# Performance work log

Measured on AMD Instinct MI355X. Metric: run time of the kernel, lower is better.

## Reference

```python
import jax, jax.numpy as jnp
import numpy as np


def setup_inputs() -> dict:
    key = jax.random.key(0)
    k1, k2, k3, k4 = jax.random.split(key, 4)
    n_nodes, n_edges, d_in, d_half = 100000, 1600000, 256, 128
    x = jax.random.normal(k1, (n_nodes, d_in), dtype=jnp.float32)
    edge_index = jax.random.randint(k2, (2, n_edges), 0, n_nodes, dtype=jnp.int64)
    W_f = jax.random.normal(k3, (d_half, d_in), dtype=jnp.float32) * (1.0 / np.sqrt(d_in))
    W_b = jax.random.normal(k4, (d_half, d_in), dtype=jnp.float32) * (1.0 / np.sqrt(d_in))
    bias_param = jnp.zeros((2 * d_half,), dtype=jnp.float32)
    return {"x": x, "edge_index": edge_index, "W_f": W_f, "W_b": W_b, "bias_param": bias_param}


def _inv_sqrt(deg):
    # deg.pow(-0.5) with inf -> 0
    return jnp.where(deg > 0, jax.lax.rsqrt(deg), 0.0)


def reference(x, edge_index, W_f, W_b, bias_param):
    n_nodes = x.shape[0]
    # add_remaining_self_loops with fill value 1
    loops = jnp.arange(n_nodes, dtype=edge_index.dtype)
    ei = jnp.concatenate([edge_index, jnp.stack([loops, loops])], axis=1)
    n_e = ei.shape[1]
    w = jnp.ones((n_e,), dtype=x.dtype)
    # directed_norm, flow='source_to_target': col, row = edge_index
    col, row = ei[0], ei[1]
    in_deg = jax.ops.segment_sum(w, col, num_segments=n_nodes)
    out_deg = jax.ops.segment_sum(w, row, num_segments=n_nodes)
    ew = _inv_sqrt(out_deg)[row] * w * _inv_sqrt(in_deg)[col]  # [E]
    # adj_forward: source=row, target=col ; adj_backward: source=col, target=row
    mf = (x @ W_f.T)[row] * ew[:, None]           # [E, d_half]
    y_forward = jax.ops.segment_sum(mf, col, num_segments=n_nodes)
    mb = (x @ W_b.T)[col] * ew[:, None]           # [E, d_half]
    y_backward = jax.ops.segment_sum(mb, row, num_segments=n_nodes)
    y = jnp.concatenate([y_forward, y_backward], axis=-1) + bias_param
    return y
```

## Files before the change

### kernel.cpp

```cpp
#include <hip/hip_runtime.h>

#define D_IN 256
#define D_HALF 128

typedef __attribute__((ext_vector_type(8))) short short8;
typedef __attribute__((ext_vector_type(4))) float float4v;

__device__ __forceinline__ unsigned short f2bf(float f) {
    union { float f; unsigned u; } v; v.f = f;
    unsigned r = v.u + 0x7FFF + ((v.u >> 16) & 1);
    return (unsigned short)(r >> 16);
}
__device__ __forceinline__ float bflo(unsigned u) { union { unsigned u; float f; } v; v.u = u << 16; return v.f; }
__device__ __forceinline__ float bfhi(unsigned u) { union { unsigned u; float f; } v; v.u = u & 0xffff0000u; return v.f; }

__device__ __forceinline__ void async16(const void* g, void* l) {
    __builtin_amdgcn_global_load_lds(
        (const __attribute__((address_space(1))) unsigned int*)g,
        (__attribute__((address_space(3))) unsigned int*)l, 16, 0, 0);
}


#define S_SH 8
#define NBK_MAX 1024
#define CAP 4608
#define EPB 4096

__global__ void p1_cast_kernel(const int* __restrict__ col, const int* __restrict__ row,
                               int* __restrict__ gcnt, unsigned* __restrict__ staging,
                               int N, int E, int nP1,
                               const float* __restrict__ x, const float* __restrict__ Wf,
                               const float* __restrict__ Wb, unsigned short* __restrict__ xb,
                               unsigned short* __restrict__ wcat, int n4) {
    __shared__ int hist[NBK_MAX];
    __shared__ int base_[NBK_MAX];
    const int tid = threadIdx.x;

    if (blockIdx.x >= nP1) {
        int i = (blockIdx.x - nP1) * 256 + tid;
        const int w4 = (2 * D_HALF * D_IN) / 4;
        if (i < n4) {
            float4 v = ((const float4*)x)[i];
            ushort4 o = { f2bf(v.x), f2bf(v.y), f2bf(v.z), f2bf(v.w) };
            ((ushort4*)xb)[i] = o;
        } else if (i < n4 + w4) {
            int j = i - n4;
            int elem = j * 4;
            const float* src = (elem < D_HALF * D_IN) ? (Wf + elem) : (Wb + (elem - D_HALF * D_IN));
            float4 v = *(const float4*)src;
            ushort4 o = { f2bf(v.x), f2bf(v.y), f2bf(v.z), f2bf(v.w) };
            ((ushort4*)wcat)[j] = o;
        }
        return;
    }

    #pragma unroll
    for (int b = 0; b < NBK_MAX / 256; ++b) hist[b * 256 + tid] = 0;
    __syncthreads();

    int ce[16], re[16], rf_[16], rb_[16];
    const int e0 = blockIdx.x * EPB;
    #pragma unroll
    for (int j = 0; j < 16; ++j) {
        int e = e0 + j * 256 + tid;
        if (e < E) {
            ce[j] = col[e];
            re[j] = row[e];
            rf_[j] = atomicAdd(&hist[ce[j] >> S_SH], 1);
            rb_[j] = atomicAdd(&hist[(N + re[j]) >> S_SH], 1);
        } else {
            ce[j] = -1; re[j] = 0; rf_[j] = 0; rb_[j] = 0;
        }
    }
    __syncthreads();

    #pragma unroll
    for (int b = 0; b < NBK_MAX / 256; ++b) {
        int idx = b * 256 + tid;
        int c = hist[idx];
        if (c) base_[idx] = idx * CAP + atomicAdd(&gcnt[idx], c);
    }
    __syncthreads();

    #pragma unroll
    for (int j = 0; j < 16; ++j) {
        if (ce[j] >= 0) {
            int c = ce[j], r = re[j];
            staging[(size_t)base_[c >> S_SH] + rf_[j]] =
                ((unsigned)(c & 255) << 23) | (unsigned)r;
            int sb = N + r;
            staging[(size_t)base_[sb >> S_SH] + rb_[j]] =
                ((unsigned)(sb & 255) << 23) | (unsigned)c;
        }
    }
}

__global__ void bsort_kernel(const unsigned* __restrict__ staging, const int* __restrict__ gcnt,
                             int* __restrict__ cnt, int* __restrict__ offs,
                             float* __restrict__ inv_in, float* __restrict__ inv_out,
                             int* __restrict__ adj, int N, int M) {
    __shared__ int lcnt[256];
    __shared__ int s[256];
    __shared__ int lbuf[CAP];
    __shared__ int bc[2];
    const int tid = threadIdx.x;
    const int b = blockIdx.x;
    const int s0 = b << S_SH;

    int g0 = gcnt[4 * tid], g1 = gcnt[4 * tid + 1];
    int g2 = gcnt[4 * tid + 2], g3 = gcnt[4 * tid + 3];
    int loc = g0 + g1 + g2 + g3;
    s[tid] = loc;
    __syncthreads();
    for (int d = 1; d < 256; d <<= 1) {
        int t = (tid >= d) ? s[tid - d] : 0;
        __syncthreads();
        s[tid] += t;
        __syncthreads();
    }
    if (tid == (b >> 2)) {
        int e = s[tid] - loc;
        int r = b & 3;
        if (r > 0) e += g0;
        if (r > 1) e += g1;
        if (r > 2) e += g2;
        bc[0] = e;
        bc[1] = (r == 0) ? g0 : (r == 1) ? g1 : (r == 2) ? g2 : g3;
    }
    lcnt[tid] = 0;
    __syncthreads();

    const int base = bc[0];
    const int count = bc[1];
    const unsigned* __restrict__ st = staging + (size_t)b * CAP;

    for (int i = tid; i < count; i += 256)
        atomicAdd(&lcnt[st[i] >> 23], 1);
    __syncthreads();

    int v = lcnt[tid];
    s[tid] = v;
    __syncthreads();
    for (int d = 1; d < 256; d <<= 1) {
        int t = (tid >= d) ? s[tid - d] : 0;
        __syncthreads();
        s[tid] += t;
        __syncthreads();
    }
    int excl = s[tid] - v;

    int gs = s0 + tid;
    if (gs < M) {
        cnt[gs] = v;  offs[gs] = base + excl;
        float iv = rsqrtf((float)(v + 1));
        if (gs < N) inv_in[gs] = iv;
        else        inv_out[gs - N] = iv;
    }

    lcnt[tid] = excl;
    __syncthreads();

    for (int i = tid; i < count; i += 256) {
        unsigned it = st[i];
        int sl = it >> 23;
        int p = atomicAdd(&lcnt[sl], 1);
        lbuf[p] = (int)(it & 0x7fffffu);
    }
    __syncthreads();
    for (int i = tid; i < count; i += 256)
        adj[base + i] = lbuf[i];
}


#define BM 128
#define BN 128
#define BK 32

__global__ void gemm_mfma_kernel(const unsigned short* __restrict__ xb,
                                 const unsigned short* __restrict__ wcat,
                                 const float* __restrict__ inv_in,
                                 const float* __restrict__ inv_out,
                                 unsigned short* __restrict__ zb, int N) {
    __shared__ __align__(16) unsigned short As[BM * BK];
    __shared__ __align__(16) unsigned short Bs[BN * BK];
    const int tid = threadIdx.x;
    const int wave = tid >> 6;
    const int lane = tid & 63;
    const int bm = blockIdx.x * BM;
    const int bn = blockIdx.y * BN;
    const int warpM = wave >> 1;
    const int warpN = wave & 1;
    const int l15 = lane & 15;
    const int quad = lane >> 4;

    float4v acc[4][4];
    #pragma unroll
    for (int i = 0; i < 4; ++i)
        #pragma unroll
        for (int j = 0; j < 4; ++j)
            acc[i][j] = (float4v){0.f, 0.f, 0.f, 0.f};

    for (int kt = 0; kt < D_IN / BK; ++kt) {
        #pragma unroll
        for (int iss = 0; iss < 2; ++iss) {
            const int pbase = iss * 256 + wave * 64;
            const int p = pbase + lane;
            const int m = p >> 2;
            const int g = (p & 3) ^ ((m >> 1) & 3);
            int gm = bm + m; if (gm >= N) gm = N - 1;
            async16(xb + (size_t)gm * D_IN + kt * BK + g * 8, &As[pbase * 8]);
            async16(wcat + (size_t)(bn + m) * D_IN + kt * BK + g * 8, &Bs[pbase * 8]);
        }
        __syncthreads();

        short8 af[4], bfr[4];
        #pragma unroll
        for (int mi = 0; mi < 4; ++mi) {
            int m = warpM * 64 + mi * 16 + l15;
            af[mi] = *(const short8*)&As[m * BK + (quad ^ ((m >> 1) & 3)) * 8];
        }
        #pragma unroll
        for (int ni = 0; ni < 4; ++ni) {
            int n = warpN * 64 + ni * 16 + l15;
            bfr[ni] = *(const short8*)&Bs[n * BK + (quad ^ ((n >> 1) & 3)) * 8];
        }
        #pragma unroll
        for (int mi = 0; mi < 4; ++mi)
            #pragma unroll
            for (int ni = 0; ni < 4; ++ni)
                acc[mi][ni] = __builtin_amdgcn_mfma_f32_16x16x32_bf16(af[mi], bfr[ni], acc[mi][ni], 0, 0, 0);
        __syncthreads();
    }

    const float* __restrict__ sc = (blockIdx.y == 0) ? inv_out : inv_in;
    #pragma unroll
    for (int mi = 0; mi < 4; ++mi) {
        #pragma unroll
        for (int reg = 0; reg < 4; ++reg) {
            int gm = bm + warpM * 64 + mi * 16 + quad * 4 + reg;
            if (gm < N) {
                float s = sc[gm];
                #pragma unroll
                for (int ni = 0; ni < 4; ++ni) {
                    int gn = bn + warpN * 64 + ni * 16 + l15;
                    zb[(size_t)gm * D_IN + gn] = f2bf(acc[mi][ni][reg] * s);
                }
            }
        }
    }
}


__global__ void gather_kernel(const unsigned short* __restrict__ zb, const int* __restrict__ adj,
                              const int* __restrict__ offs, const int* __restrict__ cnt,
                              const float* __restrict__ inv_in, const float* __restrict__ inv_out,
                              const float* __restrict__ bias,
                              float* __restrict__ out, int N) {
    const int wave = threadIdx.x >> 6;
    const int lane = threadIdx.x & 63;
    const int slot = blockIdx.x * 4 + wave;
    if (slot >= 2 * N) return;
    const int dir = (slot >= N) ? 1 : 0;
    const int node = slot - dir * N;
    const int beg = offs[slot];
    const int deg = cnt[slot];
    const int end = beg + deg;
    const int g4 = lane >> 4;
    const int l15 = lane & 15;
    const int chu = dir * D_HALF + 8 * l15;
    const int pa = g4 << 2;

    float a0 = 0.f, a1 = 0.f, a2 = 0.f, a3 = 0.f;
    float a4 = 0.f, a5 = 0.f, a6 = 0.f, a7 = 0.f;

    for (int base = beg; base < end; base += 64) {
        int len = end - base; if (len > 64) len = 64;
        int nb = (lane < len) ? adj[base + lane] : node;
        #pragma unroll 8
        for (int j0 = 0; j0 < len; j0 += 4) {
            int nsel = __builtin_amdgcn_ds_bpermute((j0 << 2) + pa, nb);
            float m = (j0 + g4 < len) ? 1.0f : 0.0f;
            const uint4 u = *(const uint4*)&zb[(size_t)nsel * D_IN + chu];
            a0 = fmaf(m, bflo(u.x), a0); a1 = fmaf(m, bfhi(u.x), a1);
            a2 = fmaf(m, bflo(u.y), a2); a3 = fmaf(m, bfhi(u.y), a3);
            a4 = fmaf(m, bflo(u.z), a4); a5 = fmaf(m, bfhi(u.z), a5);
            a6 = fmaf(m, bflo(u.w), a6); a7 = fmaf(m, bfhi(u.w), a7);
        }
    }

    a0 += __shfl_xor(a0, 16); a0 += __shfl_xor(a0, 32);
    a1 += __shfl_xor(a1, 16); a1 += __shfl_xor(a1, 32);
    a2 += __shfl_xor(a2, 16); a2 += __shfl_xor(a2, 32);
    a3 += __shfl_xor(a3, 16); a3 += __shfl_xor(a3, 32);
    a4 += __shfl_xor(a4, 16); a4 += __shfl_xor(a4, 32);
    a5 += __shfl_xor(a5, 16); a5 += __shfl_xor(a5, 32);
    a6 += __shfl_xor(a6, 16); a6 += __shfl_xor(a6, 32);
    a7 += __shfl_xor(a7, 16); a7 += __shfl_xor(a7, 32);

    if (g4 == 0) {
        const uint4 us = *(const uint4*)&zb[(size_t)node * D_IN + chu];
        a0 += bflo(us.x); a1 += bfhi(us.x);
        a2 += bflo(us.y); a3 += bfhi(us.y);
        a4 += bflo(us.z); a5 += bfhi(us.z);
        a6 += bflo(us.w); a7 += bfhi(us.w);

        const float scale = dir ? inv_out[node] : inv_in[node];
        const float4 bv0 = *(const float4*)&bias[chu];
        const float4 bv1 = *(const float4*)&bias[chu + 4];
        size_t oi = (size_t)node * D_IN + chu;
        float4 o0 = { bv0.x + scale * a0, bv0.y + scale * a1,
                      bv0.z + scale * a2, bv0.w + scale * a3 };
        float4 o1 = { bv1.x + scale * a4, bv1.y + scale * a5,
                      bv1.z + scale * a6, bv1.w + scale * a7 };
        *(float4*)&out[oi] = o0;
        *(float4*)&out[oi + 4] = o1;
    }
}


extern "C" void kernel_launch(void* const* d_in, const int* in_sizes, int n_in,
                              void* d_out, int out_size, void* d_ws, size_t ws_size,
                              hipStream_t stream) {
    const float* x    = (const float*)d_in[0];
    const int*   ei   = (const int*)d_in[1];
    const float* Wf   = (const float*)d_in[2];
    const float* Wb   = (const float*)d_in[3];
    const float* bias = (const float*)d_in[4];
    float* out = (float*)d_out;

    const int N = in_sizes[0] / D_IN;
    const int E = in_sizes[1] / 2;
    const int* col = ei;
    const int* rowp = ei + E;

    char* ws = (char*)d_ws;
    unsigned short* xb = (unsigned short*)ws;   ws += (size_t)N * D_IN * sizeof(short);
    unsigned short* zb = (unsigned short*)ws;   ws += (size_t)N * D_IN * sizeof(short);
    unsigned short* wcat = (unsigned short*)ws; ws += (size_t)2 * D_HALF * D_IN * sizeof(short);
    int* cnt = (int*)ws;            ws += (size_t)2 * N * sizeof(int);
    int* offs = (int*)ws;           ws += (size_t)2 * N * sizeof(int);
    float* inv_in = (float*)ws;     ws += (size_t)N * sizeof(float);
    float* inv_out = (float*)ws;    ws += (size_t)N * sizeof(float);
    int* adj = (int*)ws;            ws += (size_t)2 * E * sizeof(int);
    int* gcnt = (int*)ws;           ws += NBK_MAX * sizeof(int);

    unsigned* staging = (unsigned*)zb;

    const int M = 2 * N;
    const int nbuck = (M + 255) >> S_SH;
    const int nP1 = (E + EPB - 1) / EPB;
    const int n4 = N * D_IN / 4;
    const int w4 = (2 * D_HALF * D_IN) / 4;
    const int nCast = (n4 + w4 + 255) / 256;

    hipMemsetAsync(gcnt, 0, NBK_MAX * sizeof(int), stream);
    p1_cast_kernel<<<nP1 + nCast, 256, 0, stream>>>(col, rowp, gcnt, staging, N, E, nP1,
                                                    x, Wf, Wb, xb, wcat, n4);
    bsort_kernel<<<nbuck, 256, 0, stream>>>(staging, gcnt, cnt, offs, inv_in, inv_out, adj, N, M);

    gemm_mfma_kernel<<<dim3((N + BM - 1) / BM, D_IN / BN), 256, 0, stream>>>(xb, wcat, inv_in, inv_out, zb, N);

    gather_kernel<<<(2 * N + 3) / 4, 256, 0, stream>>>(zb, adj, offs, cnt, inv_in, inv_out, bias, out, N);
}
```

Before: 377.7 us.

## Locally sort bucketed edges in LDS before writing staging for coalesced stores

The bucketing pass now handles each block's 4096 edges in two rounds of 2048. Each round builds a local bucket histogram, prefix-scans it, and places the packed entries into a bucket-sorted shared buffer. A strided loop then copies that buffer to global staging, so consecutive threads write consecutive addresses within a bucket instead of scattering. This adds a block scan, extra barriers and more shared memory per block, which may reduce occupancy.

```diff
diff --git a/kernel.cpp b/kernel.cpp
--- a/kernel.cpp
+++ b/kernel.cpp
@@ -25,6 +25,7 @@
 #define NBK_MAX 1024
 #define CAP 4608
 #define EPB 4096
+#define RND 2048
 
 __global__ void p1_cast_kernel(const int* __restrict__ col, const int* __restrict__ row,
                                int* __restrict__ gcnt, unsigned* __restrict__ staging,
@@ -34,6 +35,10 @@
                                unsigned short* __restrict__ wcat, int n4) {
     __shared__ int hist[NBK_MAX];
     __shared__ int base_[NBK_MAX];
+    __shared__ int lstart[NBK_MAX];
+    __shared__ int s[256];
+    __shared__ unsigned lbuf[2 * RND];
+    __shared__ unsigned short lbk[2 * RND];
     const int tid = threadIdx.x;
 
     if (blockIdx.x >= nP1) {
@@ -54,44 +59,72 @@
         return;
     }
 
-    #pragma unroll
-    for (int b = 0; b < NBK_MAX / 256; ++b) hist[b * 256 + tid] = 0;
-    __syncthreads();
-
-    int ce[16], re[16], rf_[16], rb_[16];
-    const int e0 = blockIdx.x * EPB;
-    #pragma unroll
-    for (int j = 0; j < 16; ++j) {
-        int e = e0 + j * 256 + tid;
-        if (e < E) {
-            ce[j] = col[e];
-            re[j] = row[e];
-            rf_[j] = atomicAdd(&hist[ce[j] >> S_SH], 1);
-            rb_[j] = atomicAdd(&hist[(N + re[j]) >> S_SH], 1);
-        } else {
-            ce[j] = -1; re[j] = 0; rf_[j] = 0; rb_[j] = 0;
-        }
-    }
-    __syncthreads();
-
-    #pragma unroll
-    for (int b = 0; b < NBK_MAX / 256; ++b) {
-        int idx = b * 256 + tid;
-        int c = hist[idx];
-        if (c) base_[idx] = idx * CAP + atomicAdd(&gcnt[idx], c);
-    }
-    __syncthreads();
-
-    #pragma unroll
-    for (int j = 0; j < 16; ++j) {
-        if (ce[j] >= 0) {
-            int c = ce[j], r = re[j];
-            staging[(size_t)base_[c >> S_SH] + rf_[j]] =
-                ((unsigned)(c & 255) << 23) | (unsigned)r;
-            int sb = N + r;
-            staging[(size_t)base_[sb >> S_SH] + rb_[j]] =
-                ((unsigned)(sb & 255) << 23) | (unsigned)c;
-        }
+    for (int rnd = 0; rnd < 2; ++rnd) {
+        #pragma unroll
+        for (int b = 0; b < NBK_MAX / 256; ++b) hist[b * 256 + tid] = 0;
+        __syncthreads();
+
+        int ce[8], re[8], rf_[8], rb_[8];
+        const int e0 = blockIdx.x * EPB + rnd * RND;
+        #pragma unroll
+        for (int j = 0; j < 8; ++j) {
+            int e = e0 + j * 256 + tid;
+            if (e < E) {
+                ce[j] = col[e];
+                re[j] = row[e];
+                rf_[j] = atomicAdd(&hist[ce[j] >> S_SH], 1);
+                rb_[j] = atomicAdd(&hist[(N + re[j]) >> S_SH], 1);
+            } else {
+                ce[j] = -1; re[j] = 0; rf_[j] = 0; rb_[j] = 0;
+            }
+        }
+        __syncthreads();
+
+        int c0 = hist[4 * tid], c1 = hist[4 * tid + 1];
+        int c2 = hist[4 * tid + 2], c3 = hist[4 * tid + 3];
+        if (c0) base_[4 * tid]     = (4 * tid) * CAP     + atomicAdd(&gcnt[4 * tid], c0);
+        if (c1) base_[4 * tid + 1] = (4 * tid + 1) * CAP + atomicAdd(&gcnt[4 * tid + 1], c1);
+        if (c2) base_[4 * tid + 2] = (4 * tid + 2) * CAP + atomicAdd(&gcnt[4 * tid + 2], c2);
+        if (c3) base_[4 * tid + 3] = (4 * tid + 3) * CAP + atomicAdd(&gcnt[4 * tid + 3], c3);
+        int loc = c0 + c1 + c2 + c3;
+        s[tid] = loc;
+        __syncthreads();
+        for (int d = 1; d < 256; d <<= 1) {
+            int t = (tid >= d) ? s[tid - d] : 0;
+            __syncthreads();
+            s[tid] += t;
+            __syncthreads();
+        }
+        int excl = s[tid] - loc;
+        lstart[4 * tid] = excl;
+        lstart[4 * tid + 1] = excl + c0;
+        lstart[4 * tid + 2] = excl + c0 + c1;
+        lstart[4 * tid + 3] = excl + c0 + c1 + c2;
+        __syncthreads();
+        const int total = s[255];
+
+        #pragma unroll
+        for (int j = 0; j < 8; ++j) {
+            if (ce[j] >= 0) {
+                int c = ce[j], r = re[j];
+                int bf = c >> S_SH;
+                int pf = lstart[bf] + rf_[j];
+                lbuf[pf] = ((unsigned)(c & 255) << 23) | (unsigned)r;
+                lbk[pf] = (unsigned short)bf;
+                int sb = N + r;
+                int bb = sb >> S_SH;
+                int pb = lstart[bb] + rb_[j];
+                lbuf[pb] = ((unsigned)(sb & 255) << 23) | (unsigned)c;
+                lbk[pb] = (unsigned short)bb;
+            }
+        }
+        __syncthreads();
+
+        for (int i = tid; i < total; i += 256) {
+            int bk = lbk[i];
+            staging[(size_t)base_[bk] + (i - lstart[bk])] = lbuf[i];
+        }
+        __syncthreads();
     }
 }
 
```

Measured after the change: 407.4 us. 7.9% more time.
